# Kernel tuning notes

Measured on AMD Instinct MI355X. Metric: run time of the kernel, lower is better.

Reference implementation:

```python
import jax, jax.numpy as jnp
import numpy as np

EPS = 1e-12  # matches torch F.normalize default eps

def _l2_normalize(x):
    # F.normalize: x / max(||x||, eps)
    n = jnp.linalg.norm(x, axis=-1, keepdims=True)
    return x / jnp.maximum(n, EPS)

def setup_inputs() -> dict:
    key = jax.random.key(0)
    k1, k2 = jax.random.split(key)
    sat = jax.random.normal(k1, (256, 64, 128), dtype=jnp.float32)   # [b, j, d]
    pano = jax.random.normal(k2, (64, 64, 128), dtype=jnp.float32)   # [a, i, d]
    return {"sat_embeddings_unnormalized": sat,
            "pano_embeddings_unnormalized": pano}

def reference(sat_embeddings_unnormalized, pano_embeddings_unnormalized):
    pano_n = _l2_normalize(pano_embeddings_unnormalized)  # [a, i, d]
    sat_n = _l2_normalize(sat_embeddings_unnormalized)    # [b, j, d]
    # similarity: [a, b, i, j]
    sim = jnp.einsum('aid,bjd->abij', pano_n, sat_n)
    # maxsim: max over sat tokens (j), sum over pano tokens (i) -> [a, b]
    return sim.max(axis=3).sum(axis=2)
```

## Files before the change

### kernel.cpp

```cpp
#include <hip/hip_runtime.h>
#include <hip/hip_bf16.h>


typedef __bf16 bf16x8 __attribute__((ext_vector_type(8)));
typedef float  f32x16 __attribute__((ext_vector_type(16)));
typedef unsigned int u32;

__device__ __forceinline__ void gload16(const void* g, void* l) {
    __builtin_amdgcn_global_load_lds((const __attribute__((address_space(1))) u32*)g,
                                     (__attribute__((address_space(3))) u32*)l, 16, 0, 0);
}

__device__ __forceinline__ unsigned short f2bf_rne(float x) {
    u32 u = __builtin_bit_cast(u32, x);
    return (unsigned short)((u + 0x7FFFu + ((u >> 16) & 1u)) >> 16);
}

__global__ __launch_bounds__(256) void normalize_all(
        const float* __restrict__ sat, const float* __restrict__ pano,
        unsigned short* __restrict__ satN, unsigned short* __restrict__ panoN) {
    int row  = blockIdx.x * 8 + (threadIdx.x >> 5);
    int lane = threadIdx.x & 31;
    const float* src;
    unsigned short* dst;
    if (row < 16384) { src = sat  + (size_t)row * 128;           dst = satN  + (size_t)row * 128; }
    else             { src = pano + (size_t)(row - 16384) * 128; dst = panoN + (size_t)(row - 16384) * 128; }
    const float4 v = *reinterpret_cast<const float4*>(src + lane * 4);
    float ss = v.x * v.x + v.y * v.y + v.z * v.z + v.w * v.w;
    #pragma unroll
    for (int m = 16; m >= 1; m >>= 1) ss += __shfl_xor(ss, m);
    float sc = 1.0f / fmaxf(sqrtf(ss), 1e-12f);
    ushort4 o;
    o.x = f2bf_rne(v.x * sc); o.y = f2bf_rne(v.y * sc);
    o.z = f2bf_rne(v.z * sc); o.w = f2bf_rne(v.w * sc);
    *reinterpret_cast<ushort4*>(dst + lane * 4) = o;
}

__global__ __launch_bounds__(256, 2) void maxsim_kernel(
        const unsigned short* __restrict__ satN,
        const unsigned short* __restrict__ panoN,
        float* __restrict__ out) {
    __shared__ unsigned short Slds[4][128 * 64];

    const int tid  = threadIdx.x;
    const int wid  = tid >> 6;
    const int lane = tid & 63;
    const int rl   = lane & 31;
    const int hi   = lane >> 5;

    const int bid = blockIdx.x;
    const int swz = (bid & 7) * 64 + (bid >> 3);
    const int jg  = swz >> 5;
    const int it  = swz & 31;

    const int wm = wid >> 1;
    const int wn = wid & 1;

    bf16x8 bfr[2][8];
    {
        const unsigned short* pb =
            panoN + ((size_t)(it * 128 + wn * 64 + rl)) * 128 + hi * 8;
        #pragma unroll
        for (int n = 0; n < 2; ++n)
            #pragma unroll
            for (int ks = 0; ks < 8; ++ks)
                bfr[n][ks] = *reinterpret_cast<const bf16x8*>(pb + (size_t)n * 32 * 128 + ks * 16);
    }

#define STAGE(h_) do {                                                          \
    const char* gb_ = (const char*)satN                                         \
        + ((size_t)(jg * 1024 + ((h_) >> 1) * 128)) * 256 + ((h_) & 1) * 128;   \
    char* lb_ = (char*)&Slds[(h_) & 3][0];                                      \
    _Pragma("unroll")                                                           \
    for (int i_ = 0; i_ < 4; ++i_) {                                            \
        int P_ = (wid * 4 + i_) * 1024 + lane * 16;                             \
        int r_ = P_ >> 7;                                                       \
        int g_ = ((P_ >> 4) & 7) ^ (r_ & 7);                                    \
        gload16(gb_ + (size_t)r_ * 256 + g_ * 16, lb_ + P_);                    \
    } } while (0)

#define COMPUTE(h_, koff_) do {                                                 \
    const char* sb_ = (const char*)&Slds[(h_) & 3][0];                          \
    __builtin_amdgcn_s_setprio(1);                                              \
    _Pragma("unroll")                                                           \
    for (int ks = 0; ks < 4; ++ks) {                                            \
        bf16x8 a_[2];                                                           \
        _Pragma("unroll")                                                       \
        for (int m = 0; m < 2; ++m) {                                           \
            int row = wm * 64 + m * 32 + rl;                                    \
            a_[m] = *(const bf16x8*)(sb_ + row * 128 + ((((ks << 1) | hi) ^ (row & 7)) << 4)); \
        }                                                                       \
        _Pragma("unroll")                                                       \
        for (int m = 0; m < 2; ++m)                                             \
            _Pragma("unroll")                                                   \
            for (int n = 0; n < 2; ++n)                                         \
                acc[m][n] = __builtin_amdgcn_mfma_f32_32x32x16_bf16(            \
                    a_[m], bfr[n][(koff_) + ks], acc[m][n], 0, 0, 0);           \
    }                                                                           \
    __builtin_amdgcn_s_setprio(0);                                              \
} while (0)

#define SYNC(N_) do {                                                           \
    asm volatile("s_waitcnt vmcnt(" #N_ ")" ::: "memory");                      \
    __builtin_amdgcn_s_barrier();                                               \
    __builtin_amdgcn_sched_barrier(0);                                          \
} while (0)

#define EPILOGUE(t_) do {                                                       \
    float v0 = acc[0][0][0], v1 = acc[0][1][0];                                 \
    _Pragma("unroll")                                                           \
    for (int m = 0; m < 2; ++m)                                                 \
        _Pragma("unroll")                                                       \
        for (int q = 0; q < 16; ++q) {                                          \
            if (m == 0 && q == 0) continue;                                     \
            v0 = fmaxf(v0, acc[m][0][q]);                                       \
            v1 = fmaxf(v1, acc[m][1][q]);                                       \
        }                                                                       \
    v0 = fmaxf(v0, __shfl_xor(v0, 32));                                         \
    v1 = fmaxf(v1, __shfl_xor(v1, 32));                                         \
    float s_ = v0 + v1;                                                         \
    _Pragma("unroll")                                                           \
    for (int d_ = 1; d_ <= 16; d_ <<= 1) s_ += __shfl_xor(s_, d_);              \
    if (lane == 0) out[(it * 2 + wn) * 256 + (jg * 16 + (t_) * 2 + wm)] = s_;   \
    _Pragma("unroll")                                                           \
    for (int m = 0; m < 2; ++m)                                                 \
        _Pragma("unroll")                                                       \
        for (int n = 0; n < 2; ++n)                                             \
            _Pragma("unroll")                                                   \
            for (int q = 0; q < 16; ++q) acc[m][n][q] = 0.f;                    \
} while (0)

    STAGE(0); STAGE(1); STAGE(2);

    f32x16 acc[2][2];
    #pragma unroll
    for (int m = 0; m < 2; ++m)
        #pragma unroll
        for (int n = 0; n < 2; ++n)
            #pragma unroll
            for (int q = 0; q < 16; ++q) acc[m][n][q] = 0.f;

    #pragma unroll 1
    for (int t = 0; t < 7; ++t) {
        const int h0 = 2 * t;
        SYNC(8);
        STAGE(h0 + 3);
        __builtin_amdgcn_sched_barrier(0);
        COMPUTE(h0, 0);

        SYNC(8);
        if (t < 6) STAGE(h0 + 4);
        __builtin_amdgcn_sched_barrier(0);
        COMPUTE(h0 + 1, 4);

        EPILOGUE(t);
    }
    SYNC(4);
    COMPUTE(14, 0);
    SYNC(0);
    COMPUTE(15, 4);
    EPILOGUE(7);

#undef STAGE
#undef COMPUTE
#undef SYNC
#undef EPILOGUE
}

extern "C" void kernel_launch(void* const* d_in, const int* in_sizes, int n_in,
                              void* d_out, int out_size, void* d_ws, size_t ws_size,
                              hipStream_t stream) {
    const float* sat  = (const float*)d_in[0];
    const float* pano = (const float*)d_in[1];
    float* out = (float*)d_out;

    unsigned short* panoN = (unsigned short*)d_ws;
    unsigned short* satN  = panoN + (size_t)4096 * 128;

    normalize_all<<<2560, 256, 0, stream>>>(sat, pano, satN, panoN);
    maxsim_kernel<<<512, 256, 0, stream>>>(satN, panoN, out);
}
```

Measured before the change: 29.83 us.

## Fuse L2 normalization into the maxsim kernel and drop the separate normalize pass

Removes the standalone normalize kernel and its bf16 workspace. The maxsim kernel now reads fp32 pano rows and normalizes them into bf16 MFMA fragments in registers. Each block also loads fp32 sat tiles into registers, normalizes them, and writes swizzled bf16 into a double-buffered LDS area, overlapping the next tile's global loads with the current epilogue. This saves a kernel launch and the workspace write/read round trip. In exchange, every block redundantly normalizes the same sat rows and reads twice as many bytes (fp32 instead of bf16) from L2. The async global-to-LDS prefetch pipeline is also replaced by register staging with one barrier per tile.

```diff
diff --git a/kernel.cpp b/kernel.cpp
--- a/kernel.cpp
+++ b/kernel.cpp
@@ -5,103 +5,109 @@
 typedef __bf16 bf16x8 __attribute__((ext_vector_type(8)));
 typedef float  f32x16 __attribute__((ext_vector_type(16)));
 typedef unsigned int u32;
+typedef u32 u32x4 __attribute__((ext_vector_type(4)));
 
-__device__ __forceinline__ void gload16(const void* g, void* l) {
-    __builtin_amdgcn_global_load_lds((const __attribute__((address_space(1))) u32*)g,
-                                     (__attribute__((address_space(3))) u32*)l, 16, 0, 0);
+__device__ __forceinline__ u32 pkbf16(float a, float b) {
+    u32 r;
+    asm("v_cvt_pk_bf16_f32 %0, %1, %2" : "=v"(r) : "v"(a), "v"(b));
+    return r;
 }
 
-__device__ __forceinline__ unsigned short f2bf_rne(float x) {
-    u32 u = __builtin_bit_cast(u32, x);
-    return (unsigned short)((u + 0x7FFFu + ((u >> 16) & 1u)) >> 16);
-}
-
-__global__ __launch_bounds__(256) void normalize_all(
-        const float* __restrict__ sat, const float* __restrict__ pano,
-        unsigned short* __restrict__ satN, unsigned short* __restrict__ panoN) {
-    int row  = blockIdx.x * 8 + (threadIdx.x >> 5);
-    int lane = threadIdx.x & 31;
-    const float* src;
-    unsigned short* dst;
-    if (row < 16384) { src = sat  + (size_t)row * 128;           dst = satN  + (size_t)row * 128; }
-    else             { src = pano + (size_t)(row - 16384) * 128; dst = panoN + (size_t)(row - 16384) * 128; }
-    const float4 v = *reinterpret_cast<const float4*>(src + lane * 4);
-    float ss = v.x * v.x + v.y * v.y + v.z * v.z + v.w * v.w;
-    #pragma unroll
-    for (int m = 16; m >= 1; m >>= 1) ss += __shfl_xor(ss, m);
-    float sc = 1.0f / fmaxf(sqrtf(ss), 1e-12f);
-    ushort4 o;
-    o.x = f2bf_rne(v.x * sc); o.y = f2bf_rne(v.y * sc);
-    o.z = f2bf_rne(v.z * sc); o.w = f2bf_rne(v.w * sc);
-    *reinterpret_cast<ushort4*>(dst + lane * 4) = o;
-}
-
-__global__ __launch_bounds__(256, 2) void maxsim_kernel(
-        const unsigned short* __restrict__ satN,
-        const unsigned short* __restrict__ panoN,
+__global__ __launch_bounds__(256, 2) void fused_maxsim(
+        const float* __restrict__ satF, const float* __restrict__ panoF,
         float* __restrict__ out) {
-    __shared__ unsigned short Slds[4][128 * 64];
+    __shared__ unsigned char Slds[2][32768];
 
     const int tid  = threadIdx.x;
     const int wid  = tid >> 6;
     const int lane = tid & 63;
     const int rl   = lane & 31;
     const int hi   = lane >> 5;
+    const int rl16 = lane & 15;
+    const int q4   = lane >> 4;
 
     const int bid = blockIdx.x;
     const int swz = (bid & 7) * 64 + (bid >> 3);
     const int jg  = swz >> 5;
     const int it  = swz & 31;
-
-    const int wm = wid >> 1;
-    const int wn = wid & 1;
+    const int wm  = wid >> 1;
+    const int wn  = wid & 1;
 
     bf16x8 bfr[2][8];
-    {
-        const unsigned short* pb =
-            panoN + ((size_t)(it * 128 + wn * 64 + rl)) * 128 + hi * 8;
+    #pragma unroll
+    for (int n = 0; n < 2; ++n) {
+        const float* pr = panoF + (size_t)(it * 128 + wn * 64 + n * 32 + rl) * 128 + hi * 8;
+        float4 f[16];
         #pragma unroll
-        for (int n = 0; n < 2; ++n)
-            #pragma unroll
-            for (int ks = 0; ks < 8; ++ks)
-                bfr[n][ks] = *reinterpret_cast<const bf16x8*>(pb + (size_t)n * 32 * 128 + ks * 16);
+        for (int ks = 0; ks < 8; ++ks) {
+            f[2*ks]   = *(const float4*)(pr + ks * 16);
+            f[2*ks+1] = *(const float4*)(pr + ks * 16 + 4);
+        }
+        float ss = 0.f;
+        #pragma unroll
+        for (int i = 0; i < 16; ++i)
+            ss += f[i].x*f[i].x + f[i].y*f[i].y + f[i].z*f[i].z + f[i].w*f[i].w;
+        ss += __shfl_xor(ss, 32);
+        float sc = 1.0f / fmaxf(sqrtf(ss), 1e-12f);
+        #pragma unroll
+        for (int ks = 0; ks < 8; ++ks) {
+            u32x4 w;
+            w[0] = pkbf16(f[2*ks].x*sc,   f[2*ks].y*sc);
+            w[1] = pkbf16(f[2*ks].z*sc,   f[2*ks].w*sc);
+            w[2] = pkbf16(f[2*ks+1].x*sc, f[2*ks+1].y*sc);
+            w[3] = pkbf16(f[2*ks+1].z*sc, f[2*ks+1].w*sc);
+            bfr[n][ks] = __builtin_bit_cast(bf16x8, w);
+        }
     }
 
-#define STAGE(h_) do {                                                          \
-    const char* gb_ = (const char*)satN                                         \
-        + ((size_t)(jg * 1024 + ((h_) >> 1) * 128)) * 256 + ((h_) & 1) * 128;   \
-    char* lb_ = (char*)&Slds[(h_) & 3][0];                                      \
-    _Pragma("unroll")                                                           \
-    for (int i_ = 0; i_ < 4; ++i_) {                                            \
-        int P_ = (wid * 4 + i_) * 1024 + lane * 16;                             \
-        int r_ = P_ >> 7;                                                       \
-        int g_ = ((P_ >> 4) & 7) ^ (r_ & 7);                                    \
-        gload16(gb_ + (size_t)r_ * 256 + g_ * 16, lb_ + P_);                    \
-    } } while (0)
+#define SATLOAD(t_, fA_, fB_) do {                                              \
+    const float* s0_ = satF + (size_t)(jg*1024 + (t_)*128 + wid*16 + rl16) * 128 + q4*32; \
+    const float* s1_ = s0_ + 64 * 128;                                          \
+    _Pragma("unroll") for (int i = 0; i < 8; ++i) fA_[i] = *(const float4*)(s0_ + i*4); \
+    _Pragma("unroll") for (int i = 0; i < 8; ++i) fB_[i] = *(const float4*)(s1_ + i*4); \
+} while (0)
 
-#define COMPUTE(h_, koff_) do {                                                 \
-    const char* sb_ = (const char*)&Slds[(h_) & 3][0];                          \
+#define SATNORM(f_, R_, b_) do {                                                \
+    float ss_ = 0.f;                                                            \
+    _Pragma("unroll") for (int i = 0; i < 8; ++i)                               \
+        ss_ += f_[i].x*f_[i].x + f_[i].y*f_[i].y + f_[i].z*f_[i].z + f_[i].w*f_[i].w; \
+    ss_ += __shfl_xor(ss_, 16); ss_ += __shfl_xor(ss_, 32);                     \
+    float sc_ = 1.0f / fmaxf(sqrtf(ss_), 1e-12f);                               \
+    char* lb_ = (char*)&Slds[b_][0];                                            \
+    _Pragma("unroll") for (int j = 0; j < 4; ++j) {                             \
+        int cg_ = q4*4 + j, h_ = cg_ >> 3, c_ = cg_ & 7;                        \
+        u32x4 w_;                                                               \
+        w_[0] = pkbf16(f_[2*j].x*sc_,   f_[2*j].y*sc_);                         \
+        w_[1] = pkbf16(f_[2*j].z*sc_,   f_[2*j].w*sc_);                         \
+        w_[2] = pkbf16(f_[2*j+1].x*sc_, f_[2*j+1].y*sc_);                       \
+        w_[3] = pkbf16(f_[2*j+1].z*sc_, f_[2*j+1].w*sc_);                       \
+        *(u32x4*)(lb_ + h_*16384 + (R_)*128 + ((c_ ^ ((R_) & 7)) << 4)) = w_;   \
+    }                                                                           \
+} while (0)
+
+#define COMPUTE(b_, h_, koff_) do {                                             \
+    const char* sb_ = (const char*)&Slds[b_][0] + (h_) * 16384;                 \
     __builtin_amdgcn_s_setprio(1);                                              \
     _Pragma("unroll")                                                           \
     for (int ks = 0; ks < 4; ++ks) {                                            \
         bf16x8 a_[2];                                                           \
         _Pragma("unroll")                                                       \
         for (int m = 0; m < 2; ++m) {                                           \
-            int row = wm * 64 + m * 32 + rl;                                    \
-            a_[m] = *(const bf16x8*)(sb_ + row * 128 + ((((ks << 1) | hi) ^ (row & 7)) << 4)); \
+            int row = wm*64 + m*32 + rl;                                        \
+            a_[m] = *(const bf16x8*)(sb_ + row*128 + ((((ks<<1)|hi) ^ (row & 7)) << 4)); \
         }                                                                       \
         _Pragma("unroll")                                                       \
         for (int m = 0; m < 2; ++m)                                             \
             _Pragma("unroll")                                                   \
             for (int n = 0; n < 2; ++n)                                         \
                 acc[m][n] = __builtin_amdgcn_mfma_f32_32x32x16_bf16(            \
-                    a_[m], bfr[n][(koff_) + ks], acc[m][n], 0, 0, 0);           \
+                    a_[m], bfr[n][(koff_)+ks], acc[m][n], 0, 0, 0);             \
     }                                                                           \
     __builtin_amdgcn_s_setprio(0);                                              \
 } while (0)
 
-#define SYNC(N_) do {                                                           \
-    asm volatile("s_waitcnt vmcnt(" #N_ ")" ::: "memory");                      \
+#define PUBLISH() do {                                                          \
+    asm volatile("s_waitcnt lgkmcnt(0)" ::: "memory");                          \
     __builtin_amdgcn_s_barrier();                                               \
     __builtin_amdgcn_sched_barrier(0);                                          \
 } while (0)
@@ -122,48 +128,46 @@
     _Pragma("unroll")                                                           \
     for (int d_ = 1; d_ <= 16; d_ <<= 1) s_ += __shfl_xor(s_, d_);              \
     if (lane == 0) out[(it * 2 + wn) * 256 + (jg * 16 + (t_) * 2 + wm)] = s_;   \
-    _Pragma("unroll")                                                           \
-    for (int m = 0; m < 2; ++m)                                                 \
-        _Pragma("unroll")                                                       \
-        for (int n = 0; n < 2; ++n)                                             \
-            _Pragma("unroll")                                                   \
-            for (int q = 0; q < 16; ++q) acc[m][n][q] = 0.f;                    \
 } while (0)
 
-    STAGE(0); STAGE(1); STAGE(2);
-
-    f32x16 acc[2][2];
-    #pragma unroll
-    for (int m = 0; m < 2; ++m)
-        #pragma unroll
-        for (int n = 0; n < 2; ++n)
-            #pragma unroll
-            for (int q = 0; q < 16; ++q) acc[m][n][q] = 0.f;
+    {
+        float4 fA[8], fB[8];
+        SATLOAD(0, fA, fB);
+        SATNORM(fA, wid*16 + rl16, 0);
+        SATNORM(fB, 64 + wid*16 + rl16, 0);
+        PUBLISH();
+    }
 
     #pragma unroll 1
-    for (int t = 0; t < 7; ++t) {
-        const int h0 = 2 * t;
-        SYNC(8);
-        STAGE(h0 + 3);
-        __builtin_amdgcn_sched_barrier(0);
-        COMPUTE(h0, 0);
+    for (int t = 0; t < 8; ++t) {
+        f32x16 acc[2][2];
+        #pragma unroll
+        for (int m = 0; m < 2; ++m)
+            #pragma unroll
+            for (int n = 0; n < 2; ++n)
+                #pragma unroll
+                for (int q = 0; q < 16; ++q) acc[m][n][q] = 0.f;
 
-        SYNC(8);
-        if (t < 6) STAGE(h0 + 4);
-        __builtin_amdgcn_sched_barrier(0);
-        COMPUTE(h0 + 1, 4);
+        COMPUTE(t & 1, 0, 0);
+        COMPUTE(t & 1, 1, 4);
+
+        float4 fA[8], fB[8];
+        const bool more = (t < 7);
+        if (more) SATLOAD(t + 1, fA, fB);
 
         EPILOGUE(t);
+
+        if (more) {
+            SATNORM(fA, wid*16 + rl16, (t + 1) & 1);
+            SATNORM(fB, 64 + wid*16 + rl16, (t + 1) & 1);
+            PUBLISH();
+        }
     }
-    SYNC(4);
-    COMPUTE(14, 0);
-    SYNC(0);
-    COMPUTE(15, 4);
-    EPILOGUE(7);
 
-#undef STAGE
+#undef SATLOAD
+#undef SATNORM
 #undef COMPUTE
-#undef SYNC
+#undef PUBLISH
 #undef EPILOGUE
 }
 
@@ -174,9 +178,5 @@
     const float* pano = (const float*)d_in[1];
     float* out = (float*)d_out;
 
-    unsigned short* panoN = (unsigned short*)d_ws;
-    unsigned short* satN  = panoN + (size_t)4096 * 128;
-
-    normalize_all<<<2560, 256, 0, stream>>>(sat, pano, satN, panoN);
-    maxsim_kernel<<<512, 256, 0, stream>>>(satN, panoN, out);
+    fused_maxsim<<<512, 256, 0, stream>>>(sat, pano, out);
 }
```

Result: slower. 52.86 us (+77.2%).
